# Optimization experiments

Hardware: AMD Instinct MI355X
Metric: run time of the kernel (lower is better)

Reference implementation:

```python
import jax, jax.numpy as jnp
import numpy as np

N_QUBITS = 8
N_LAYERS = 1
DIM = 1 << N_QUBITS  # 256 statevector amplitudes; PennyLane wire 0 = most significant bit

_idx = np.arange(DIM)
_BITS = np.stack([(_idx >> (N_QUBITS - 1 - w)) & 1 for w in range(N_QUBITS)])  # (n, D)
_FLIP = np.stack([_idx ^ (1 << (N_QUBITS - 1 - w)) for w in range(N_QUBITS)])  # (n, D)

def _cnot_perm(c, t):
    return _idx ^ (((_idx >> (N_QUBITS - 1 - c)) & 1) << (N_QUBITS - 1 - t))

_CNOT_NP = [_cnot_perm(w, w + 1) for w in range(N_QUBITS - 1)] + [_cnot_perm(N_QUBITS - 1, 0)]
BITS = jnp.asarray(_BITS)
FLIP = jnp.asarray(_FLIP)
CNOTS = [jnp.asarray(p) for p in _CNOT_NP]


def _ry(t):
    c = jnp.cos(t / 2)
    s = jnp.sin(t / 2)
    return jnp.stack([jnp.stack([c, -s], -1), jnp.stack([s, c], -1)], -2).astype(jnp.complex64)


def _rx(t):
    c = jnp.cos(t / 2).astype(jnp.complex64)
    s = (-1j) * jnp.sin(t / 2).astype(jnp.complex64)
    return jnp.stack([jnp.stack([c, s], -1), jnp.stack([s, c], -1)], -2)


def _rz(t):
    tc = t.astype(jnp.complex64)
    e0 = jnp.exp(-0.5j * tc)
    e1 = jnp.exp(0.5j * tc)
    z = jnp.zeros_like(e0)
    return jnp.stack([jnp.stack([e0, z], -1), jnp.stack([z, e1], -1)], -2)


def _apply(state, U, w):
    # state: (B, 2**n) complex64; U: (2,2) shared or (B,2,2) per-sample; wire w (MSB-first)
    B = state.shape[0]
    s = state.reshape(B, 1 << w, 2, -1)
    if U.ndim == 3:
        s = jnp.einsum('bij,bajc->baic', U, s)
    else:
        s = jnp.einsum('ij,bajc->baic', U, s)
    return s.reshape(B, DIM)


def _circuit(angles, weights):
    # angles: (B, n_qubits) float32; weights: (n_layers, n_qubits, 3) float32
    B = angles.shape[0]
    state = jnp.zeros((B, DIM), jnp.complex64).at[:, 0].set(1.0)
    for w in range(N_QUBITS):
        state = _apply(state, _ry(angles[:, w]), w)  # per-sample RY encoding
    for l in range(N_LAYERS):
        for w in range(N_QUBITS):
            state = _apply(state, _rx(weights[l, w, 0]), w)
            state = _apply(state, _ry(weights[l, w, 1]), w)
            state = _apply(state, _rz(weights[l, w, 2]), w)
        for p in CNOTS:  # CNOT ring entangler as basis permutation
            state = state[:, p]
    probs = jnp.abs(state) ** 2
    outs = []
    for w in range(N_QUBITS):
        overlap = jnp.conj(state) * state[:, FLIP[w]]
        sign = (1.0 - 2.0 * BITS[w]).astype(probs.dtype)
        outs.append(jnp.sum(jnp.real(overlap), -1))       # <X_w>
        outs.append(jnp.sum(sign * jnp.imag(overlap), -1))  # <Y_w>
        outs.append(jnp.sum(sign * probs, -1))            # <Z_w>
    return jnp.stack(outs, -1)  # (B, 3*n_qubits), order X0,Y0,Z0,X1,...


def setup_inputs() -> dict:
    key = jax.random.key(0)
    k1, k2, k3 = jax.random.split(key, 3)
    B, IN_DIM = 16384, 512
    h = jax.random.normal(k1, (B, IN_DIM), jnp.float32)
    W_pre = 0.02 * jax.random.normal(k2, (N_QUBITS, IN_DIM), jnp.float32)
    b_pre = jnp.zeros((N_QUBITS,), jnp.float32)
    weights = 0.01 * jax.random.normal(k3, (N_LAYERS, N_QUBITS, 3), jnp.float32)
    return {"h": h, "W_pre": W_pre, "b_pre": b_pre, "weights": weights}


def reference(h, W_pre, b_pre, weights):
    a = h @ W_pre.T + b_pre
    a = jnp.clip(jnp.tanh(a) * (jnp.pi / 2), -jnp.pi, jnp.pi)  # _scale_to_angles
    z = _circuit(a, weights)
    norm = jnp.linalg.norm(z, axis=-1, keepdims=True)
    return z / jnp.maximum(norm, 1e-12)  # F.normalize(dim=-1)
```

## Files before the change

kernel.cpp:

```cpp
#include <hip/hip_runtime.h>


__device__ const unsigned int OMASK[24] = {
  0x00000003u,
  0x00FC0201u,
  0x00FE0000u,
  0x00000006u,
  0x00010204u,
  0x00030000u,
  0x0000000Cu,
  0x00030408u,
  0x00070000u,
  0x00000018u,
  0x00070810u,
  0x000F0000u,
  0x00000030u,
  0x000F1020u,
  0x001F0000u,
  0x00000060u,
  0x001F2040u,
  0x003F0000u,
  0x000000C0u,
  0x003F4080u,
  0x007F0000u,
  0x00000083u,
  0x807C8300u,
  0x00FF0000u
};

__global__ __launch_bounds__(256) void vqc_kernel(
    const float* __restrict__ h,
    const float* __restrict__ Wp,
    const float* __restrict__ bp,
    const float* __restrict__ wt,
    float* __restrict__ out,
    int B)
{
    const int lane  = threadIdx.x & 63;
    const int wave  = (blockIdx.x * blockDim.x + threadIdx.x) >> 6;
    const int nwv   = (gridDim.x * blockDim.x) >> 6;
    const int u     = lane >> 3;

    const float4* W4 = (const float4*)Wp;
    float wf[8][8];
    #pragma unroll
    for (int q = 0; q < 8; ++q) {
        float4 v0 = W4[q * 128 + lane * 2 + 0];
        float4 v1 = W4[q * 128 + lane * 2 + 1];
        wf[q][0] = v0.x; wf[q][1] = v0.y; wf[q][2] = v0.z; wf[q][3] = v0.w;
        wf[q][4] = v1.x; wf[q][5] = v1.y; wf[q][6] = v1.z; wf[q][7] = v1.w;
    }
    const float bias = bp[u];

    float t0 = wt[u * 3 + 0] * 0.5f;
    float t1 = wt[u * 3 + 1] * 0.5f;
    float t2 = wt[u * 3 + 2] * 0.5f;
    float s0, c0, s1, c1, sz, cz;
    __sincosf(t0, &s0, &c0);
    __sincosf(t1, &s1, &c1);
    __sincosf(t2, &sz, &cz);
    const float N00r =  c1 * c0, N00i =  s1 * s0;
    const float N01r = -s1 * c0, N01i = -c1 * s0;
    const float N10r =  s1 * c0, N10i = -c1 * s0;
    const float N11r =  c1 * c0, N11i = -s1 * s0;
    const float M00r = cz * N00r + sz * N00i, M00i = cz * N00i - sz * N00r;
    const float M01r = cz * N01r + sz * N01i, M01i = cz * N01i - sz * N01r;
    const float M10r = cz * N10r - sz * N10i, M10i = cz * N10i + sz * N10r;
    const float M11r = cz * N11r - sz * N11i, M11i = cz * N11i + sz * N11r;

    const unsigned int omask = OMASK[lane < 24 ? lane : 0];

    const float4* H4 = (const float4*)h;
    const int R = (B + nwv - 1) / nwv;
    const int row0 = wave * R;

    for (int r = 0; r < R; ++r) {
        const int row = row0 + r;
        if (row >= B) break;

        float4 h0 = H4[row * 128 + lane * 2 + 0];
        float4 h1 = H4[row * 128 + lane * 2 + 1];
        float hf[8] = { h0.x, h0.y, h0.z, h0.w, h1.x, h1.y, h1.z, h1.w };
        float acc[8];
        #pragma unroll
        for (int q = 0; q < 8; ++q) {
            float a = 0.f;
            #pragma unroll
            for (int j = 0; j < 8; ++j) a = fmaf(wf[q][j], hf[j], a);
            acc[q] = a;
        }
        #pragma unroll
        for (int q = 0; q < 8; ++q) {
            acc[q] += __shfl_xor(acc[q], 8);
            acc[q] += __shfl_xor(acc[q], 16);
            acc[q] += __shfl_xor(acc[q], 32);
        }
        float v = acc[0];
        #pragma unroll
        for (int q = 1; q < 8; ++q) v = (u == q) ? acc[q] : v;
        v += __shfl_xor(v, 1);
        v += __shfl_xor(v, 2);
        v += __shfl_xor(v, 4);

        float a = v + bias;
        a = fminf(fmaxf(a, -10.f), 10.f);
        float e = __expf(a + a);
        float th = (e - 1.f) / (e + 1.f);
        float phi = th * 0.78539816339744831f;
        float ss, cc;
        __sincosf(phi, &ss, &cc);
        float ar = M00r * cc + M01r * ss, ai = M00i * cc + M01i * ss;
        float br = M10r * cc + M11r * ss, bi = M10i * cc + M11i * ss;
        float Zv = (ar * ar + ai * ai) - (br * br + bi * bi);
        float Xv = 2.f * (ar * br + ai * bi);
        float Yv = 2.f * (ar * bi - ai * br);

        float Xs[8], Ys[8], Zs[8];
        #pragma unroll
        for (int q = 0; q < 8; ++q) {
            Xs[q] = __shfl(Xv, q * 8);
            Ys[q] = __shfl(Yv, q * 8);
            Zs[q] = __shfl(Zv, q * 8);
        }

        float val = 1.f;
        #pragma unroll
        for (int q = 0; q < 8; ++q) {
            float f = 1.f;
            if (omask & (1u       << q)) f = Xs[q];
            if (omask & (0x100u   << q)) f = Ys[q];
            if (omask & (0x10000u << q)) f = Zs[q];
            val *= f;
        }
        if (omask & 0x80000000u) val = -val;

        float sq = (lane < 24) ? val * val : 0.f;
        sq += __shfl_xor(sq, 1);
        sq += __shfl_xor(sq, 2);
        sq += __shfl_xor(sq, 4);
        sq += __shfl_xor(sq, 8);
        sq += __shfl_xor(sq, 16);
        float nrm = fmaxf(sqrtf(sq), 1e-12f);
        float o = val / nrm;

        if (lane < 24) out[row * 24 + lane] = o;
    }
}

extern "C" void kernel_launch(void* const* d_in, const int* in_sizes, int n_in,
                              void* d_out, int out_size, void* d_ws, size_t ws_size,
                              hipStream_t stream) {
    const float* h  = (const float*)d_in[0];
    const float* Wp = (const float*)d_in[1];
    const float* bp = (const float*)d_in[2];
    const float* wt = (const float*)d_in[3];
    float* out = (float*)d_out;

    const int B = in_sizes[0] / 512;
    const int nblk = 1024;
    vqc_kernel<<<nblk, 256, 0, stream>>>(h, Wp, bp, wt, out, B);
}
```

Before: 84.81 us.

## Split into GEMV and per-row epilogue kernels with transpose-style shuffle reduction

The single fused kernel becomes two. The first computes the 8 pre-activations for two rows per wave, using a butterfly transpose-reduction that swaps partial sums instead of fully reducing all 8 accumulators, and writes them to the workspace. The second runs one thread per row: it computes the closed-form X/Y/Z products with prefix and suffix Z products and writes the output with float4 stores. This removes the per-row cross-lane shuffles and OMASK lookups, at the cost of a second launch and a small workspace round-trip. The tanh clamp also moves from 10 to 15.

```diff
diff --git a/kernel.cpp b/kernel.cpp
--- a/kernel.cpp
+++ b/kernel.cpp
@@ -1,45 +1,15 @@
 #include <hip/hip_runtime.h>
 
 
-__device__ const unsigned int OMASK[24] = {
-  0x00000003u,
-  0x00FC0201u,
-  0x00FE0000u,
-  0x00000006u,
-  0x00010204u,
-  0x00030000u,
-  0x0000000Cu,
-  0x00030408u,
-  0x00070000u,
-  0x00000018u,
-  0x00070810u,
-  0x000F0000u,
-  0x00000030u,
-  0x000F1020u,
-  0x001F0000u,
-  0x00000060u,
-  0x001F2040u,
-  0x003F0000u,
-  0x000000C0u,
-  0x003F4080u,
-  0x007F0000u,
-  0x00000083u,
-  0x807C8300u,
-  0x00FF0000u
-};
-
-__global__ __launch_bounds__(256) void vqc_kernel(
+__global__ __launch_bounds__(256) void vqc_gemv(
     const float* __restrict__ h,
     const float* __restrict__ Wp,
-    const float* __restrict__ bp,
-    const float* __restrict__ wt,
-    float* __restrict__ out,
+    float* __restrict__ aw,
     int B)
 {
-    const int lane  = threadIdx.x & 63;
-    const int wave  = (blockIdx.x * blockDim.x + threadIdx.x) >> 6;
-    const int nwv   = (gridDim.x * blockDim.x) >> 6;
-    const int u     = lane >> 3;
+    const int lane = threadIdx.x & 63;
+    const int wave = (blockIdx.x * blockDim.x + threadIdx.x) >> 6;
+    const int nwv  = (gridDim.x * blockDim.x) >> 6;
 
     const float4* W4 = (const float4*)Wp;
     float wf[8][8];
@@ -50,60 +20,110 @@
         wf[q][0] = v0.x; wf[q][1] = v0.y; wf[q][2] = v0.z; wf[q][3] = v0.w;
         wf[q][4] = v1.x; wf[q][5] = v1.y; wf[q][6] = v1.z; wf[q][7] = v1.w;
     }
-    const float bias = bp[u];
 
-    float t0 = wt[u * 3 + 0] * 0.5f;
-    float t1 = wt[u * 3 + 1] * 0.5f;
-    float t2 = wt[u * 3 + 2] * 0.5f;
-    float s0, c0, s1, c1, sz, cz;
-    __sincosf(t0, &s0, &c0);
-    __sincosf(t1, &s1, &c1);
-    __sincosf(t2, &sz, &cz);
-    const float N00r =  c1 * c0, N00i =  s1 * s0;
-    const float N01r = -s1 * c0, N01i = -c1 * s0;
-    const float N10r =  s1 * c0, N10i = -c1 * s0;
-    const float N11r =  c1 * c0, N11i = -s1 * s0;
-    const float M00r = cz * N00r + sz * N00i, M00i = cz * N00i - sz * N00r;
-    const float M01r = cz * N01r + sz * N01i, M01i = cz * N01i - sz * N01r;
-    const float M10r = cz * N10r - sz * N10i, M10i = cz * N10i + sz * N10r;
-    const float M11r = cz * N11r - sz * N11i, M11i = cz * N11i + sz * N11r;
+    const int b3 = (lane >> 3) & 1, b4 = (lane >> 4) & 1, b5 = (lane >> 5) & 1;
+    const float4* H4 = (const float4*)h;
 
-    const unsigned int omask = OMASK[lane < 24 ? lane : 0];
+    const int row0 = wave * 2;
+    if (row0 >= B) return;
 
-    const float4* H4 = (const float4*)h;
-    const int R = (B + nwv - 1) / nwv;
-    const int row0 = wave * R;
+    float4 h00 = H4[row0 * 128 + lane * 2 + 0];
+    float4 h01 = H4[row0 * 128 + lane * 2 + 1];
+    int row1 = row0 + 1;
+    float4 h10 = H4[(row1 < B ? row1 : row0) * 128 + lane * 2 + 0];
+    float4 h11 = H4[(row1 < B ? row1 : row0) * 128 + lane * 2 + 1];
 
-    for (int r = 0; r < R; ++r) {
-        const int row = row0 + r;
-        if (row >= B) break;
+    float hf0[8] = { h00.x, h00.y, h00.z, h00.w, h01.x, h01.y, h01.z, h01.w };
+    float hf1[8] = { h10.x, h10.y, h10.z, h10.w, h11.x, h11.y, h11.z, h11.w };
 
-        float4 h0 = H4[row * 128 + lane * 2 + 0];
-        float4 h1 = H4[row * 128 + lane * 2 + 1];
-        float hf[8] = { h0.x, h0.y, h0.z, h0.w, h1.x, h1.y, h1.z, h1.w };
-        float acc[8];
+    float acc0[8], acc1[8];
+    #pragma unroll
+    for (int q = 0; q < 8; ++q) {
+        float a0 = 0.f, a1 = 0.f;
         #pragma unroll
-        for (int q = 0; q < 8; ++q) {
-            float a = 0.f;
-            #pragma unroll
-            for (int j = 0; j < 8; ++j) a = fmaf(wf[q][j], hf[j], a);
-            acc[q] = a;
+        for (int j = 0; j < 8; ++j) {
+            a0 = fmaf(wf[q][j], hf0[j], a0);
+            a1 = fmaf(wf[q][j], hf1[j], a1);
         }
-        #pragma unroll
-        for (int q = 0; q < 8; ++q) {
-            acc[q] += __shfl_xor(acc[q], 8);
-            acc[q] += __shfl_xor(acc[q], 16);
-            acc[q] += __shfl_xor(acc[q], 32);
-        }
-        float v = acc[0];
-        #pragma unroll
-        for (int q = 1; q < 8; ++q) v = (u == q) ? acc[q] : v;
-        v += __shfl_xor(v, 1);
-        v += __shfl_xor(v, 2);
-        v += __shfl_xor(v, 4);
+        acc0[q] = a0; acc1[q] = a1;
+    }
 
-        float a = v + bias;
-        a = fminf(fmaxf(a, -10.f), 10.f);
+    float n0[4], n1[4];
+    #pragma unroll
+    for (int j = 0; j < 4; ++j) {
+        float k0 = b3 ? acc0[1 + 2*j] : acc0[0 + 2*j];
+        float s0 = b3 ? acc0[0 + 2*j] : acc0[1 + 2*j];
+        float k1 = b3 ? acc1[1 + 2*j] : acc1[0 + 2*j];
+        float s1 = b3 ? acc1[0 + 2*j] : acc1[1 + 2*j];
+        n0[j] = k0 + __shfl_xor(s0, 8);
+        n1[j] = k1 + __shfl_xor(s1, 8);
+    }
+    float m0[2], m1[2];
+    #pragma unroll
+    for (int i = 0; i < 2; ++i) {
+        float k0 = b4 ? n0[1 + 2*i] : n0[0 + 2*i];
+        float s0 = b4 ? n0[0 + 2*i] : n0[1 + 2*i];
+        float k1 = b4 ? n1[1 + 2*i] : n1[0 + 2*i];
+        float s1 = b4 ? n1[0 + 2*i] : n1[1 + 2*i];
+        m0[i] = k0 + __shfl_xor(s0, 16);
+        m1[i] = k1 + __shfl_xor(s1, 16);
+    }
+    float v0, v1;
+    {
+        float k0 = b5 ? m0[1] : m0[0];
+        float s0 = b5 ? m0[0] : m0[1];
+        float k1 = b5 ? m1[1] : m1[0];
+        float s1 = b5 ? m1[0] : m1[1];
+        v0 = k0 + __shfl_xor(s0, 32);
+        v1 = k1 + __shfl_xor(s1, 32);
+    }
+    v0 += __shfl_xor(v0, 1); v1 += __shfl_xor(v1, 1);
+    v0 += __shfl_xor(v0, 2); v1 += __shfl_xor(v1, 2);
+    v0 += __shfl_xor(v0, 4); v1 += __shfl_xor(v1, 4);
+
+    if ((lane & 7) == 0) {
+        int q = lane >> 3;
+        aw[row0 * 8 + q] = v0;
+        if (row1 < B) aw[row1 * 8 + q] = v1;
+    }
+}
+
+__global__ __launch_bounds__(256) void vqc_epilogue(
+    const float* __restrict__ aw,
+    const float* __restrict__ bp,
+    const float* __restrict__ wt,
+    float* __restrict__ out,
+    int B)
+{
+    const int row = blockIdx.x * blockDim.x + threadIdx.x;
+    if (row >= B) return;
+
+    const float4* A4 = (const float4*)aw;
+    float4 a0 = A4[row * 2 + 0];
+    float4 a1 = A4[row * 2 + 1];
+    float av[8] = { a0.x, a0.y, a0.z, a0.w, a1.x, a1.y, a1.z, a1.w };
+
+    float X[8], Y[8], Z[8];
+    #pragma unroll
+    for (int q = 0; q < 8; ++q) {
+        float t0 = wt[q * 3 + 0] * 0.5f;
+        float t1 = wt[q * 3 + 1] * 0.5f;
+        float t2 = wt[q * 3 + 2] * 0.5f;
+        float s0, c0, s1, c1, sz, cz;
+        __sincosf(t0, &s0, &c0);
+        __sincosf(t1, &s1, &c1);
+        __sincosf(t2, &sz, &cz);
+        float N00r =  c1 * c0, N00i =  s1 * s0;
+        float N01r = -s1 * c0, N01i = -c1 * s0;
+        float N10r =  s1 * c0, N10i = -c1 * s0;
+        float N11r =  c1 * c0, N11i = -s1 * s0;
+        float M00r = cz * N00r + sz * N00i, M00i = cz * N00i - sz * N00r;
+        float M01r = cz * N01r + sz * N01i, M01i = cz * N01i - sz * N01r;
+        float M10r = cz * N10r - sz * N10i, M10i = cz * N10i + sz * N10r;
+        float M11r = cz * N11r - sz * N11i, M11i = cz * N11i + sz * N11r;
+
+        float a = av[q] + bp[q];
+        a = fminf(fmaxf(a, -15.f), 15.f);
         float e = __expf(a + a);
         float th = (e - 1.f) / (e + 1.f);
         float phi = th * 0.78539816339744831f;
@@ -111,39 +131,43 @@
         __sincosf(phi, &ss, &cc);
         float ar = M00r * cc + M01r * ss, ai = M00i * cc + M01i * ss;
         float br = M10r * cc + M11r * ss, bi = M10i * cc + M11i * ss;
-        float Zv = (ar * ar + ai * ai) - (br * br + bi * bi);
-        float Xv = 2.f * (ar * br + ai * bi);
-        float Yv = 2.f * (ar * bi - ai * br);
+        Z[q] = (ar * ar + ai * ai) - (br * br + bi * bi);
+        X[q] = 2.f * (ar * br + ai * bi);
+        Y[q] = 2.f * (ar * bi - ai * br);
+    }
 
-        float Xs[8], Ys[8], Zs[8];
-        #pragma unroll
-        for (int q = 0; q < 8; ++q) {
-            Xs[q] = __shfl(Xv, q * 8);
-            Ys[q] = __shfl(Yv, q * 8);
-            Zs[q] = __shfl(Zv, q * 8);
-        }
+    float P[8], T[8];
+    P[0] = Z[0];
+    #pragma unroll
+    for (int w = 1; w < 8; ++w) P[w] = P[w - 1] * Z[w];
+    T[7] = Z[7];
+    #pragma unroll
+    for (int w = 6; w >= 0; --w) T[w] = Z[w] * T[w + 1];
+    float Z2to6 = Z[2] * Z[3] * Z[4] * Z[5] * Z[6];
 
-        float val = 1.f;
-        #pragma unroll
-        for (int q = 0; q < 8; ++q) {
-            float f = 1.f;
-            if (omask & (1u       << q)) f = Xs[q];
-            if (omask & (0x100u   << q)) f = Ys[q];
-            if (omask & (0x10000u << q)) f = Zs[q];
-            val *= f;
-        }
-        if (omask & 0x80000000u) val = -val;
+    float o[24];
+    #pragma unroll
+    for (int w = 0; w < 7; ++w) o[3 * w] = X[w] * X[w + 1];
+    o[21] = X[7] * X[0] * X[1];
+    o[1] = X[0] * Y[1] * T[2];
+    #pragma unroll
+    for (int w = 1; w < 7; ++w) o[3 * w + 1] = Y[w] * X[w + 1] * P[w - 1];
+    o[22] = -Y[7] * Y[0] * Y[1] * Z2to6;
+    o[2] = T[1];
+    #pragma unroll
+    for (int w = 1; w < 8; ++w) o[3 * w + 2] = P[w];
 
-        float sq = (lane < 24) ? val * val : 0.f;
-        sq += __shfl_xor(sq, 1);
-        sq += __shfl_xor(sq, 2);
-        sq += __shfl_xor(sq, 4);
-        sq += __shfl_xor(sq, 8);
-        sq += __shfl_xor(sq, 16);
-        float nrm = fmaxf(sqrtf(sq), 1e-12f);
-        float o = val / nrm;
+    float sq = 0.f;
+    #pragma unroll
+    for (int j = 0; j < 24; ++j) sq = fmaf(o[j], o[j], sq);
+    float inv = 1.f / fmaxf(sqrtf(sq), 1e-12f);
 
-        if (lane < 24) out[row * 24 + lane] = o;
+    float4* O4 = (float4*)(out + row * 24);
+    #pragma unroll
+    for (int j = 0; j < 6; ++j) {
+        float4 vv = { o[4 * j] * inv, o[4 * j + 1] * inv,
+                      o[4 * j + 2] * inv, o[4 * j + 3] * inv };
+        O4[j] = vv;
     }
 }
 
@@ -155,8 +179,10 @@
     const float* bp = (const float*)d_in[2];
     const float* wt = (const float*)d_in[3];
     float* out = (float*)d_out;
+    float* aw  = (float*)d_ws;
 
     const int B = in_sizes[0] / 512;
-    const int nblk = 1024;
-    vqc_kernel<<<nblk, 256, 0, stream>>>(h, Wp, bp, wt, out, B);
+    const int nblk1 = (B + 511) / 512;
+    vqc_gemv<<<nblk1 * 128, 256, 0, stream>>>(h, Wp, aw, B);
+    vqc_epilogue<<<(B + 255) / 256, 256, 0, stream>>>(aw, bp, wt, out, B);
 }
```

Result: no change. 83.45 us (-1.6%).
